# Optimization experiments

Measured on AMD Instinct MI355X. Metric: run time of the kernel, lower is better.

The kernel has to match this reference:

```python
import jax, jax.numpy as jnp
import numpy as np

B, S, I, H, L, O = 64, 512, 128, 1024, 3, 128


def _gru_cell(x, h, Wx, Wh, bh):
    # Wx: [3, H, in], Wh: [3, H, H], bh: [3, H]; gate order (z, r, g).
    # Matches: z = sig(W_xz x + W_hz h + b_z); r = sig(W_xr x + W_hr h + b_r);
    #          g = tanh(W_xg x + W_hg (r*h) + b_g); h' = z*h + (1-z)*g
    z = jax.nn.sigmoid(x @ Wx[0].T + h @ Wh[0].T + bh[0])
    r = jax.nn.sigmoid(x @ Wx[1].T + h @ Wh[1].T + bh[1])
    g = jnp.tanh(x @ Wx[2].T + (r * h) @ Wh[2].T + bh[2])
    return z * h + (1.0 - z) * g


def setup_inputs() -> dict:
    key = jax.random.key(0)
    ks = jax.random.split(key, 10)
    u = lambda k, shape, fan: jax.random.uniform(k, shape, jnp.float32, -1.0, 1.0) / np.float32(np.sqrt(fan))
    return {
        "x": jax.random.normal(ks[0], (B, S, I), jnp.float32),
        # layer 0 (input dim I)
        "Wx0": u(ks[1], (3, H, I), I),
        "Wh0": u(ks[2], (3, H, H), H),
        "bh0": u(ks[3], (3, H), H),
        # layers 1..L-1 (input dim H), stacked on leading axis
        "Wxr": u(ks[4], (L - 1, 3, H, H), H),
        "Whr": u(ks[5], (L - 1, 3, H, H), H),
        "bhr": u(ks[6], (L - 1, 3, H), H),
        # output projection
        "Wout": u(ks[7], (O, H), H),
        "bout": u(ks[8], (O,), H),
    }


def reference(x, Wx0, Wh0, bh0, Wxr, Whr, bhr, Wout, bout):
    batch = x.shape[0]
    n_rest = Wxr.shape[0]
    h_init = jnp.zeros((n_rest + 1, batch, H), x.dtype)  # [L, B, H]

    def step(hs, x_t):
        new = []
        h = _gru_cell(x_t, hs[0], Wx0, Wh0, bh0)
        new.append(h)
        inp = h
        for j in range(n_rest):  # small fixed layer count
            h = _gru_cell(inp, hs[j + 1], Wxr[j], Whr[j], bhr[j])
            new.append(h)
            inp = h
        y = inp @ Wout.T + bout
        return jnp.stack(new), y

    hs_final, ys = jax.lax.scan(step, h_init, jnp.swapaxes(x, 0, 1))
    layer_output = jnp.swapaxes(ys, 0, 1)        # (B, S, O)
    hidden_state = jnp.swapaxes(hs_final, 0, 1)  # (B, L, H)
    return layer_output, hidden_state
```

## Files before the change

### kernel.cpp

```cpp
#include <hip/hip_runtime.h>


namespace {
constexpr int kB = 64, kS = 512, kI = 128, kH = 1024, kO = 128;
constexpr int kTicks = kS + 3;
constexpr size_t kBSO = (size_t)kB * kS * kO;
constexpr int kTasksA = 218, kTasksB = 96;

__device__ float g_wxt0[3 * 128 * 1024];
__device__ float g_wht0[3 * 1024 * 1024];
__device__ float g_wxtr[6 * 1024 * 1024];
__device__ float g_whtr[6 * 1024 * 1024];
__device__ float g_woutT[1024 * 128];
__device__ float g_xT[512 * 128 * 64];
__device__ float g_hbuf[2 * 3 * 1024 * 64];
__device__ float g_zT[3 * 1024 * 64];
__device__ float g_rhT[3 * 1024 * 64];
__device__ float g_gxT[3 * 1024 * 64];
__device__ float g_partA[kTasksA * 8192];
__device__ float g_partB[kTasksB * 8192];
}


__global__ void zero_hbuf() {
  g_hbuf[blockIdx.x * 256 + threadIdx.x] = 0.f;
}

__global__ __launch_bounds__(256) void transpose_k(
    const float* __restrict__ in, int sel, int R, int C) {
  float* out;
  switch (sel) {
    case 0: out = g_wxt0; break;
    case 1: out = g_wht0; break;
    case 2: out = g_wxtr; break;
    case 3: out = g_whtr; break;
    case 4: out = g_woutT; break;
    default: out = g_xT; break;
  }
  const size_t mat = (size_t)R * C;
  in += blockIdx.z * mat;
  out += blockIdx.z * mat;
  __shared__ float t[32][33];
  const int c0 = blockIdx.x * 32, r0 = blockIdx.y * 32;
  const int tx = threadIdx.x & 31, ty = threadIdx.x >> 5;
  for (int i = ty; i < 32; i += 8) {
    const int r = r0 + i, c = c0 + tx;
    if (r < R && c < C) t[i][tx] = in[(size_t)r * C + c];
  }
  __syncthreads();
  for (int i = ty; i < 32; i += 8) {
    const int c = c0 + i, r = r0 + tx;
    if (c < C && r < R) out[(size_t)c * R + r] = t[tx][i];
  }
}

__device__ __forceinline__ void load_lds16(const float* g, float* l) {
  __builtin_amdgcn_global_load_lds(
      (const __attribute__((address_space(1))) void*)g,
      (__attribute__((address_space(3))) void*)l, 16, 0, 0);
}

__global__ __launch_bounds__(512) void gemm_tasks(int phase, int tau) {
  const int id = blockIdx.x;
  const int par = tau & 1;
  const float* hb = g_hbuf + par * 196608;

  int t_l = 0, nk = 512, ldw = 1024;
  const float* inp = nullptr; const float* w = nullptr;

  if (phase == 0) {
    if (id < 48) {
      const int gate = id / 24, q = id % 24, ng = q / 3, ks = q % 3;
      t_l = tau;
      if (ks == 0) {
        inp = g_xT + (size_t)t_l * 8192; nk = 128;
        w = g_wxt0 + (size_t)gate * 131072 + ng * 128;
      } else {
        const int k0 = (ks - 1) * 512;
        inp = hb + k0 * 64;
        w = g_wht0 + (size_t)gate * 1048576 + (size_t)k0 * 1024 + ng * 128;
      }
    } else if (id < 176) {
      const int q = id - 48, l = 1 + (q >> 6);
      const int q2 = q & 63, gate = q2 >> 5, q3 = q2 & 31, ng = q3 >> 2, ks = q3 & 3;
      t_l = tau - l;
      if (ks < 2) {
        const int k0 = ks * 512;
        inp = hb + (l - 1) * 65536 + k0 * 64;
        w = g_wxtr + (size_t)((l - 1) * 3 + gate) * 1048576 + (size_t)k0 * 1024 + ng * 128;
      } else {
        const int k0 = (ks - 2) * 512;
        inp = hb + l * 65536 + k0 * 64;
        w = g_whtr + (size_t)((l - 1) * 3 + gate) * 1048576 + (size_t)k0 * 1024 + ng * 128;
      }
    } else if (id < 184) {
      const int ng = id - 176;
      t_l = tau;
      inp = g_xT + (size_t)t_l * 8192; nk = 128;
      w = g_wxt0 + (size_t)2 * 131072 + ng * 128;
    } else if (id < 216) {
      const int q = id - 184, l = 1 + (q >> 4);
      const int q2 = q & 15, ng = q2 >> 1, ks = q2 & 1;
      t_l = tau - l;
      const int k0 = ks * 512;
      inp = hb + (l - 1) * 65536 + k0 * 64;
      w = g_wxtr + (size_t)((l - 1) * 3 + 2) * 1048576 + (size_t)k0 * 1024 + ng * 128;
    } else {
      const int ks = id - 216;
      t_l = tau - 3;
      const int k0 = ks * 512;
      inp = hb + 2 * 65536 + k0 * 64;
      w = g_woutT + (size_t)k0 * 128; ldw = 128;
    }
  } else {
    const int l = id >> 5, q = id & 31, ng = q >> 2, ks = q & 3;
    t_l = tau - l;
    const int k0 = ks * 256;
    inp = g_rhT + l * 65536 + k0 * 64; nk = 256;
    w = ((l == 0) ? g_wht0 + (size_t)2 * 1048576
                  : g_whtr + (size_t)((l - 1) * 3 + 2) * 1048576) +
        (size_t)k0 * 1024 + ng * 128;
  }
  if (t_l < 0 || t_l >= kS) return;

  __shared__ float sI[64 * 64];
  __shared__ float sW[64 * 128];
  const int tid = threadIdx.x;
  const int tn = (tid & 31) * 4, tb = (tid >> 5) * 4;
  float acc[4][4] = {};

  for (int c0 = 0; c0 < nk; c0 += 64) {
#pragma unroll
    for (int u = 0; u < 2; ++u) {
      const int idx = tid + u * 512;
      load_lds16(inp + c0 * 64 + idx * 4, sI + idx * 4);
    }
#pragma unroll
    for (int u = 0; u < 4; ++u) {
      const int idx = tid + u * 512, k = idx >> 5, f = idx & 31;
      load_lds16(w + (size_t)(c0 + k) * ldw + f * 4, sW + idx * 4);
    }
    __syncthreads();
#pragma unroll 8
    for (int k = 0; k < 64; ++k) {
      const float4 a = *(const float4*)(sI + k * 64 + tb);
      const float4 wv = *(const float4*)(sW + k * 128 + tn);
      acc[0][0] += wv.x * a.x; acc[0][1] += wv.x * a.y; acc[0][2] += wv.x * a.z; acc[0][3] += wv.x * a.w;
      acc[1][0] += wv.y * a.x; acc[1][1] += wv.y * a.y; acc[1][2] += wv.y * a.z; acc[1][3] += wv.y * a.w;
      acc[2][0] += wv.z * a.x; acc[2][1] += wv.z * a.y; acc[2][2] += wv.z * a.z; acc[2][3] += wv.z * a.w;
      acc[3][0] += wv.w * a.x; acc[3][1] += wv.w * a.y; acc[3][2] += wv.w * a.z; acc[3][3] += wv.w * a.w;
    }
    __syncthreads();
  }

  float* po = ((phase == 0) ? g_partA : g_partB) + (size_t)id * 8192;
#pragma unroll
  for (int i = 0; i < 4; ++i) {
    float4 v = {acc[i][0], acc[i][1], acc[i][2], acc[i][3]};
    *(float4*)(po + (tn + i) * 64 + tb) = v;
  }
}

__global__ __launch_bounds__(256) void reduceA(
    int tau, const float* __restrict__ Bh0, const float* __restrict__ Bhr,
    const float* __restrict__ Bout, float* __restrict__ Out) {
  const int gid = blockIdx.x * 256 + threadIdx.x;
  const int b0 = (gid & 15) * 4, c = gid >> 4;
  const int par = tau & 1;
  if (c < 6144) {
    const int gate = (c >= 3072) ? 1 : 0;
    const int cc = c - gate * 3072;
    const int l = cc >> 10, n = cc & 1023;
    const int t_l = tau - l;
    if (t_l < 0 || t_l >= kS) return;
    const int ng = n >> 7, cl = n & 127;
    int base, nks;
    if (l == 0) { base = gate * 24 + ng * 3;                  nks = 3; }
    else        { base = 48 + (l - 1) * 64 + gate * 32 + ng * 4; nks = 4; }
    const float bias = (l == 0) ? Bh0[gate * 1024 + n] : Bhr[(l - 1) * 3072 + gate * 1024 + n];
    float s0 = bias, s1 = bias, s2 = bias, s3 = bias;
    for (int j = 0; j < nks; ++j) {
      const float4 p = *(const float4*)&g_partA[(size_t)(base + j) * 8192 + cl * 64 + b0];
      s0 += p.x; s1 += p.y; s2 += p.z; s3 += p.w;
    }
    const float v0 = 1.f / (1.f + expf(-s0)), v1 = 1.f / (1.f + expf(-s1));
    const float v2 = 1.f / (1.f + expf(-s2)), v3 = 1.f / (1.f + expf(-s3));
    const int off = l * 65536 + n * 64 + b0;
    if (gate == 0) {
      *(float4*)&g_zT[off] = make_float4(v0, v1, v2, v3);
    } else {
      const float4 h = *(const float4*)&g_hbuf[par * 196608 + off];
      *(float4*)&g_rhT[off] = make_float4(v0 * h.x, v1 * h.y, v2 * h.z, v3 * h.w);
    }
  } else if (c < 9216) {
    const int cc = c - 6144, l = cc >> 10, n = cc & 1023;
    const int t_l = tau - l;
    if (t_l < 0 || t_l >= kS) return;
    const int ng = n >> 7, cl = n & 127;
    int base, nks;
    if (l == 0) { base = 176 + ng;                 nks = 1; }
    else        { base = 184 + (l - 1) * 16 + ng * 2; nks = 2; }
    const float bias = (l == 0) ? Bh0[2048 + n] : Bhr[(l - 1) * 3072 + 2048 + n];
    float s0 = bias, s1 = bias, s2 = bias, s3 = bias;
    for (int j = 0; j < nks; ++j) {
      const float4 p = *(const float4*)&g_partA[(size_t)(base + j) * 8192 + cl * 64 + b0];
      s0 += p.x; s1 += p.y; s2 += p.z; s3 += p.w;
    }
    *(float4*)&g_gxT[l * 65536 + n * 64 + b0] = make_float4(s0, s1, s2, s3);
  } else {
    const int o = c - 9216, ty = tau - 3;
    if (ty < 0 || ty >= kS) return;
    const float bias = Bout[o];
    float s0 = bias, s1 = bias, s2 = bias, s3 = bias;
    for (int j = 0; j < 2; ++j) {
      const float4 p = *(const float4*)&g_partA[(size_t)(216 + j) * 8192 + o * 64 + b0];
      s0 += p.x; s1 += p.y; s2 += p.z; s3 += p.w;
    }
    Out[((size_t)(b0 + 0) * kS + ty) * kO + o] = s0;
    Out[((size_t)(b0 + 1) * kS + ty) * kO + o] = s1;
    Out[((size_t)(b0 + 2) * kS + ty) * kO + o] = s2;
    Out[((size_t)(b0 + 3) * kS + ty) * kO + o] = s3;
  }
}

__global__ __launch_bounds__(256) void reduceB(
    int tau, float* __restrict__ Out) {
  const int gid = blockIdx.x * 256 + threadIdx.x;
  const int b0 = (gid & 15) * 4, c = gid >> 4;
  const int l = c >> 10, n = c & 1023;
  const int t_l = tau - l;
  if (t_l < 0 || t_l >= kS) return;
  const int par = tau & 1;
  const int ng = n >> 7, cl = n & 127;
  const int base = l * 32 + ng * 4;
  const int off = l * 65536 + n * 64 + b0;
  float4 gs = *(const float4*)&g_gxT[off];
  for (int j = 0; j < 4; ++j) {
    const float4 p = *(const float4*)&g_partB[(size_t)(base + j) * 8192 + cl * 64 + b0];
    gs.x += p.x; gs.y += p.y; gs.z += p.z; gs.w += p.w;
  }
  const float g0 = tanhf(gs.x), g1 = tanhf(gs.y), g2 = tanhf(gs.z), g3 = tanhf(gs.w);
  const float4 z = *(const float4*)&g_zT[off];
  const float4 h = *(const float4*)&g_hbuf[par * 196608 + off];
  float4 hn;
  hn.x = z.x * h.x + (1.f - z.x) * g0;
  hn.y = z.y * h.y + (1.f - z.y) * g1;
  hn.z = z.z * h.z + (1.f - z.z) * g2;
  hn.w = z.w * h.w + (1.f - z.w) * g3;
  *(float4*)&g_hbuf[(1 - par) * 196608 + off] = hn;
  if (t_l == kS - 1) {
    Out[kBSO + ((size_t)(b0 + 0) * 3 + l) * 1024 + n] = hn.x;
    Out[kBSO + ((size_t)(b0 + 1) * 3 + l) * 1024 + n] = hn.y;
    Out[kBSO + ((size_t)(b0 + 2) * 3 + l) * 1024 + n] = hn.z;
    Out[kBSO + ((size_t)(b0 + 3) * 3 + l) * 1024 + n] = hn.w;
  }
}

extern "C" void kernel_launch(void* const* d_in, const int* in_sizes, int n_in,
                              void* d_out, int out_size, void* d_ws, size_t ws_size,
                              hipStream_t stream) {
  const float* X    = (const float*)d_in[0];
  const float* Wx0  = (const float*)d_in[1];
  const float* Wh0  = (const float*)d_in[2];
  const float* bh0  = (const float*)d_in[3];
  const float* Wxr  = (const float*)d_in[4];
  const float* Whr  = (const float*)d_in[5];
  const float* bhr  = (const float*)d_in[6];
  const float* Wout = (const float*)d_in[7];
  const float* bout = (const float*)d_in[8];
  (void)d_ws; (void)ws_size;

  if (n_in != 9 ||
      in_sizes[0] != 64 * 512 * 128 || in_sizes[1] != 3 * 1024 * 128 ||
      in_sizes[2] != 3 * 1024 * 1024 || in_sizes[3] != 3 * 1024 ||
      in_sizes[4] != 2 * 3 * 1024 * 1024 || in_sizes[5] != 2 * 3 * 1024 * 1024 ||
      in_sizes[6] != 2 * 3 * 1024 || in_sizes[7] != 128 * 1024 ||
      in_sizes[8] != 128 || out_size != 64 * 512 * 128 + 64 * 3 * 1024)
    return;

  float* out = (float*)d_out;

  hipLaunchKernelGGL(zero_hbuf, dim3(1536), dim3(256), 0, stream);
  hipLaunchKernelGGL(transpose_k, dim3(4, 32, 3),   dim3(256), 0, stream, Wx0,  0, 1024, 128);
  hipLaunchKernelGGL(transpose_k, dim3(32, 32, 3),  dim3(256), 0, stream, Wh0,  1, 1024, 1024);
  hipLaunchKernelGGL(transpose_k, dim3(32, 32, 6),  dim3(256), 0, stream, Wxr,  2, 1024, 1024);
  hipLaunchKernelGGL(transpose_k, dim3(32, 32, 6),  dim3(256), 0, stream, Whr,  3, 1024, 1024);
  hipLaunchKernelGGL(transpose_k, dim3(32, 4, 1),   dim3(256), 0, stream, Wout, 4, 128, 1024);
  hipLaunchKernelGGL(transpose_k, dim3(2048, 2, 1), dim3(256), 0, stream, X,    5, 64, 65536);

  for (int tau = 0; tau < kTicks; ++tau) {
    hipLaunchKernelGGL(gemm_tasks, dim3(kTasksA), dim3(512), 0, stream, 0, tau);
    hipLaunchKernelGGL(reduceA, dim3(584), dim3(256), 0, stream,
                       tau, bh0, bhr, bout, out);
    if (tau < kTicks - 1) {
      hipLaunchKernelGGL(gemm_tasks, dim3(kTasksB), dim3(512), 0, stream, 1, tau);
      hipLaunchKernelGGL(reduceB, dim3(192), dim3(256), 0, stream, tau, out);
    }
  }
}
```

Measured before the change: 32.70 ms.

## Split GRU step GEMMs into finer K-split tasks and fuse gate reductions

Splits the per-tick gate GEMM into a dedicated gemmA with twice as many K-split tasks (256-thread blocks, 8x4 register tiles) and a gemmB that uses 64-wide column tiles with 8-way K-splits, giving more blocks per launch on the many-CU GPU. reduceA now only computes r*h, and reduceB fuses the z gate, the input-side g partials, the recurrent g partials and the output projection reduction. This removes the intermediate zT/gxT buffers. The cost is more partial sums to write and re-read and more blocks doing redundant setup.

```diff
diff --git a/kernel.cpp b/kernel.cpp
--- a/kernel.cpp
+++ b/kernel.cpp
@@ -5,7 +5,7 @@
 constexpr int kB = 64, kS = 512, kI = 128, kH = 1024, kO = 128;
 constexpr int kTicks = kS + 3;
 constexpr size_t kBSO = (size_t)kB * kS * kO;
-constexpr int kTasksA = 218, kTasksB = 96;
+constexpr int kTasksA = 412, kTasksB = 384;
 
 __device__ float g_wxt0[3 * 128 * 1024];
 __device__ float g_wht0[3 * 1024 * 1024];
@@ -14,11 +14,9 @@
 __device__ float g_woutT[1024 * 128];
 __device__ float g_xT[512 * 128 * 64];
 __device__ float g_hbuf[2 * 3 * 1024 * 64];
-__device__ float g_zT[3 * 1024 * 64];
 __device__ float g_rhT[3 * 1024 * 64];
-__device__ float g_gxT[3 * 1024 * 64];
 __device__ float g_partA[kTasksA * 8192];
-__device__ float g_partB[kTasksB * 8192];
+__device__ float g_partB[kTasksB * 4096];
 }
 
 
@@ -60,91 +58,136 @@
       (__attribute__((address_space(3))) void*)l, 16, 0, 0);
 }
 
-__global__ __launch_bounds__(512) void gemm_tasks(int phase, int tau) {
+__global__ __launch_bounds__(256) void gemmA(int tau) {
   const int id = blockIdx.x;
   const int par = tau & 1;
   const float* hb = g_hbuf + par * 196608;
 
-  int t_l = 0, nk = 512, ldw = 1024;
+  int t_l = 0, nk = 256, ldw = 1024;
   const float* inp = nullptr; const float* w = nullptr;
 
-  if (phase == 0) {
-    if (id < 48) {
-      const int gate = id / 24, q = id % 24, ng = q / 3, ks = q % 3;
-      t_l = tau;
-      if (ks == 0) {
-        inp = g_xT + (size_t)t_l * 8192; nk = 128;
-        w = g_wxt0 + (size_t)gate * 131072 + ng * 128;
-      } else {
-        const int k0 = (ks - 1) * 512;
-        inp = hb + k0 * 64;
-        w = g_wht0 + (size_t)gate * 1048576 + (size_t)k0 * 1024 + ng * 128;
-      }
-    } else if (id < 176) {
-      const int q = id - 48, l = 1 + (q >> 6);
-      const int q2 = q & 63, gate = q2 >> 5, q3 = q2 & 31, ng = q3 >> 2, ks = q3 & 3;
-      t_l = tau - l;
-      if (ks < 2) {
-        const int k0 = ks * 512;
-        inp = hb + (l - 1) * 65536 + k0 * 64;
-        w = g_wxtr + (size_t)((l - 1) * 3 + gate) * 1048576 + (size_t)k0 * 1024 + ng * 128;
-      } else {
-        const int k0 = (ks - 2) * 512;
-        inp = hb + l * 65536 + k0 * 64;
-        w = g_whtr + (size_t)((l - 1) * 3 + gate) * 1048576 + (size_t)k0 * 1024 + ng * 128;
-      }
-    } else if (id < 184) {
-      const int ng = id - 176;
-      t_l = tau;
+  if (id < 80) {
+    const int gate = id / 40, q = id % 40, ng = q / 5, ks = q % 5;
+    t_l = tau;
+    if (ks == 0) {
       inp = g_xT + (size_t)t_l * 8192; nk = 128;
-      w = g_wxt0 + (size_t)2 * 131072 + ng * 128;
-    } else if (id < 216) {
-      const int q = id - 184, l = 1 + (q >> 4);
-      const int q2 = q & 15, ng = q2 >> 1, ks = q2 & 1;
-      t_l = tau - l;
-      const int k0 = ks * 512;
+      w = g_wxt0 + (size_t)gate * 131072 + ng * 128;
+    } else {
+      const int k0 = (ks - 1) * 256;
+      inp = hb + k0 * 64;
+      w = g_wht0 + (size_t)gate * 1048576 + (size_t)k0 * 1024 + ng * 128;
+    }
+  } else if (id < 336) {
+    const int q = id - 80, l = 1 + (q >> 7);
+    const int q2 = q & 127, gate = q2 >> 6, q3 = q2 & 63, ng = q3 >> 3, ks = q3 & 7;
+    t_l = tau - l;
+    const int k0 = (ks & 3) * 256;
+    if (ks < 4) {
       inp = hb + (l - 1) * 65536 + k0 * 64;
-      w = g_wxtr + (size_t)((l - 1) * 3 + 2) * 1048576 + (size_t)k0 * 1024 + ng * 128;
+      w = g_wxtr + (size_t)((l - 1) * 3 + gate) * 1048576 + (size_t)k0 * 1024 + ng * 128;
     } else {
-      const int ks = id - 216;
-      t_l = tau - 3;
-      const int k0 = ks * 512;
-      inp = hb + 2 * 65536 + k0 * 64;
-      w = g_woutT + (size_t)k0 * 128; ldw = 128;
-    }
-  } else {
-    const int l = id >> 5, q = id & 31, ng = q >> 2, ks = q & 3;
+      inp = hb + l * 65536 + k0 * 64;
+      w = g_whtr + (size_t)((l - 1) * 3 + gate) * 1048576 + (size_t)k0 * 1024 + ng * 128;
+    }
+  } else if (id < 344) {
+    const int ng = id - 336;
+    t_l = tau;
+    inp = g_xT + (size_t)t_l * 8192; nk = 128;
+    w = g_wxt0 + (size_t)2 * 131072 + ng * 128;
+  } else if (id < 408) {
+    const int q = id - 344, l = 1 + (q >> 5);
+    const int q2 = q & 31, ng = q2 >> 2, ks = q2 & 3;
     t_l = tau - l;
     const int k0 = ks * 256;
-    inp = g_rhT + l * 65536 + k0 * 64; nk = 256;
-    w = ((l == 0) ? g_wht0 + (size_t)2 * 1048576
-                  : g_whtr + (size_t)((l - 1) * 3 + 2) * 1048576) +
-        (size_t)k0 * 1024 + ng * 128;
+    inp = hb + (l - 1) * 65536 + k0 * 64;
+    w = g_wxtr + (size_t)((l - 1) * 3 + 2) * 1048576 + (size_t)k0 * 1024 + ng * 128;
+  } else {
+    const int ks = id - 408;
+    t_l = tau - 3;
+    const int k0 = ks * 256;
+    inp = hb + 2 * 65536 + k0 * 64;
+    w = g_woutT + (size_t)k0 * 128; ldw = 128;
   }
   if (t_l < 0 || t_l >= kS) return;
 
   __shared__ float sI[64 * 64];
   __shared__ float sW[64 * 128];
   const int tid = threadIdx.x;
-  const int tn = (tid & 31) * 4, tb = (tid >> 5) * 4;
+  const int tn = (tid & 15) * 8, tb = (tid >> 4) * 4;
+  float acc[8][4] = {};
+
+  for (int c0 = 0; c0 < nk; c0 += 64) {
+#pragma unroll
+    for (int u = 0; u < 4; ++u) {
+      const int idx = tid + u * 256;
+      load_lds16(inp + c0 * 64 + idx * 4, sI + idx * 4);
+    }
+#pragma unroll
+    for (int u = 0; u < 8; ++u) {
+      const int idx = tid + u * 256, k = idx >> 5, f = idx & 31;
+      load_lds16(w + (size_t)(c0 + k) * ldw + f * 4, sW + idx * 4);
+    }
+    __syncthreads();
+#pragma unroll 4
+    for (int k = 0; k < 64; ++k) {
+      const float4 a = *(const float4*)(sI + k * 64 + tb);
+      const float4 w0 = *(const float4*)(sW + k * 128 + tn);
+      const float4 w1 = *(const float4*)(sW + k * 128 + tn + 4);
+      acc[0][0] += w0.x * a.x; acc[0][1] += w0.x * a.y; acc[0][2] += w0.x * a.z; acc[0][3] += w0.x * a.w;
+      acc[1][0] += w0.y * a.x; acc[1][1] += w0.y * a.y; acc[1][2] += w0.y * a.z; acc[1][3] += w0.y * a.w;
+      acc[2][0] += w0.z * a.x; acc[2][1] += w0.z * a.y; acc[2][2] += w0.z * a.z; acc[2][3] += w0.z * a.w;
+      acc[3][0] += w0.w * a.x; acc[3][1] += w0.w * a.y; acc[3][2] += w0.w * a.z; acc[3][3] += w0.w * a.w;
+      acc[4][0] += w1.x * a.x; acc[4][1] += w1.x * a.y; acc[4][2] += w1.x * a.z; acc[4][3] += w1.x * a.w;
+      acc[5][0] += w1.y * a.x; acc[5][1] += w1.y * a.y; acc[5][2] += w1.y * a.z; acc[5][3] += w1.y * a.w;
+      acc[6][0] += w1.z * a.x; acc[6][1] += w1.z * a.y; acc[6][2] += w1.z * a.z; acc[6][3] += w1.z * a.w;
+      acc[7][0] += w1.w * a.x; acc[7][1] += w1.w * a.y; acc[7][2] += w1.w * a.z; acc[7][3] += w1.w * a.w;
+    }
+    __syncthreads();
+  }
+
+  float* po = g_partA + (size_t)id * 8192;
+#pragma unroll
+  for (int i = 0; i < 8; ++i) {
+    float4 v = {acc[i][0], acc[i][1], acc[i][2], acc[i][3]};
+    *(float4*)(po + (tn + i) * 64 + tb) = v;
+  }
+}
+
+__global__ __launch_bounds__(256, 2) void gemmB(int tau) {
+  const int id = blockIdx.x;
+  const int l = id >> 7;
+  const int rem = id & 127, tile = rem >> 3, ks = rem & 7;
+  const int t_l = tau - l;
+  if (t_l < 0 || t_l >= kS) return;
+  const int k0 = ks * 128;
+  const float* inp = g_rhT + l * 65536 + k0 * 64;
+  const float* w =
+      ((l == 0) ? g_wht0 + (size_t)2 * 1048576
+                : g_whtr + (size_t)((l - 1) * 3 + 2) * 1048576) +
+      (size_t)k0 * 1024 + tile * 64;
+
+  __shared__ float sI[64 * 64];
+  __shared__ float sW[64 * 64];
+  const int tid = threadIdx.x;
+  const int tn = (tid & 15) * 4, tb = (tid >> 4) * 4;
   float acc[4][4] = {};
 
-  for (int c0 = 0; c0 < nk; c0 += 64) {
-#pragma unroll
-    for (int u = 0; u < 2; ++u) {
-      const int idx = tid + u * 512;
+  for (int c0 = 0; c0 < 128; c0 += 64) {
+#pragma unroll
+    for (int u = 0; u < 4; ++u) {
+      const int idx = tid + u * 256;
       load_lds16(inp + c0 * 64 + idx * 4, sI + idx * 4);
     }
 #pragma unroll
     for (int u = 0; u < 4; ++u) {
-      const int idx = tid + u * 512, k = idx >> 5, f = idx & 31;
-      load_lds16(w + (size_t)(c0 + k) * ldw + f * 4, sW + idx * 4);
+      const int idx = tid + u * 256, k = idx >> 4, f = idx & 15;
+      load_lds16(w + (size_t)(c0 + k) * 1024 + f * 4, sW + idx * 4);
     }
     __syncthreads();
 #pragma unroll 8
     for (int k = 0; k < 64; ++k) {
       const float4 a = *(const float4*)(sI + k * 64 + tb);
-      const float4 wv = *(const float4*)(sW + k * 128 + tn);
+      const float4 wv = *(const float4*)(sW + k * 64 + tn);
       acc[0][0] += wv.x * a.x; acc[0][1] += wv.x * a.y; acc[0][2] += wv.x * a.z; acc[0][3] += wv.x * a.w;
       acc[1][0] += wv.y * a.x; acc[1][1] += wv.y * a.y; acc[1][2] += wv.y * a.z; acc[1][3] += wv.y * a.w;
       acc[2][0] += wv.z * a.x; acc[2][1] += wv.z * a.y; acc[2][2] += wv.z * a.z; acc[2][3] += wv.z * a.w;
@@ -153,7 +196,7 @@
     __syncthreads();
   }
 
-  float* po = ((phase == 0) ? g_partA : g_partB) + (size_t)id * 8192;
+  float* po = g_partB + (size_t)id * 4096;
 #pragma unroll
   for (int i = 0; i < 4; ++i) {
     float4 v = {acc[i][0], acc[i][1], acc[i][2], acc[i][3]};
@@ -162,97 +205,95 @@
 }
 
 __global__ __launch_bounds__(256) void reduceA(
+    int tau, const float* __restrict__ Bh0, const float* __restrict__ Bhr) {
+  const int gid = blockIdx.x * 256 + threadIdx.x;
+  const int b0 = (gid & 15) * 4, c = gid >> 4;
+  const int par = tau & 1;
+  const int l = c >> 10, n = c & 1023;
+  const int t_l = tau - l;
+  if (t_l < 0 || t_l >= kS) return;
+  const int ng = n >> 7, cl = n & 127;
+  int base, nks;
+  if (l == 0) { base = 40 + ng * 5; nks = 5; }
+  else        { base = 80 + (l - 1) * 128 + 64 + ng * 8; nks = 8; }
+  const float bias = (l == 0) ? Bh0[1024 + n] : Bhr[(l - 1) * 3072 + 1024 + n];
+  float s0 = bias, s1 = bias, s2 = bias, s3 = bias;
+  for (int j = 0; j < nks; ++j) {
+    const float4 p = *(const float4*)&g_partA[(size_t)(base + j) * 8192 + cl * 64 + b0];
+    s0 += p.x; s1 += p.y; s2 += p.z; s3 += p.w;
+  }
+  const float v0 = 1.f / (1.f + expf(-s0)), v1 = 1.f / (1.f + expf(-s1));
+  const float v2 = 1.f / (1.f + expf(-s2)), v3 = 1.f / (1.f + expf(-s3));
+  const int off = l * 65536 + n * 64 + b0;
+  const float4 h = *(const float4*)&g_hbuf[par * 196608 + off];
+  *(float4*)&g_rhT[off] = make_float4(v0 * h.x, v1 * h.y, v2 * h.z, v3 * h.w);
+}
+
+__global__ __launch_bounds__(256) void reduceB(
     int tau, const float* __restrict__ Bh0, const float* __restrict__ Bhr,
     const float* __restrict__ Bout, float* __restrict__ Out) {
   const int gid = blockIdx.x * 256 + threadIdx.x;
   const int b0 = (gid & 15) * 4, c = gid >> 4;
   const int par = tau & 1;
-  if (c < 6144) {
-    const int gate = (c >= 3072) ? 1 : 0;
-    const int cc = c - gate * 3072;
-    const int l = cc >> 10, n = cc & 1023;
+  if (c < 3072) {
+    const int l = c >> 10, n = c & 1023;
     const int t_l = tau - l;
     if (t_l < 0 || t_l >= kS) return;
     const int ng = n >> 7, cl = n & 127;
-    int base, nks;
-    if (l == 0) { base = gate * 24 + ng * 3;                  nks = 3; }
-    else        { base = 48 + (l - 1) * 64 + gate * 32 + ng * 4; nks = 4; }
-    const float bias = (l == 0) ? Bh0[gate * 1024 + n] : Bhr[(l - 1) * 3072 + gate * 1024 + n];
-    float s0 = bias, s1 = bias, s2 = bias, s3 = bias;
-    for (int j = 0; j < nks; ++j) {
-      const float4 p = *(const float4*)&g_partA[(size_t)(base + j) * 8192 + cl * 64 + b0];
-      s0 += p.x; s1 += p.y; s2 += p.z; s3 += p.w;
-    }
-    const float v0 = 1.f / (1.f + expf(-s0)), v1 = 1.f / (1.f + expf(-s1));
-    const float v2 = 1.f / (1.f + expf(-s2)), v3 = 1.f / (1.f + expf(-s3));
+    int zbase, znks;
+    if (l == 0) { zbase = ng * 5; znks = 5; }
+    else        { zbase = 80 + (l - 1) * 128 + ng * 8; znks = 8; }
+    const float zb = (l == 0) ? Bh0[n] : Bhr[(l - 1) * 3072 + n];
+    float z0 = zb, z1 = zb, z2 = zb, z3 = zb;
+    for (int j = 0; j < znks; ++j) {
+      const float4 p = *(const float4*)&g_partA[(size_t)(zbase + j) * 8192 + cl * 64 + b0];
+      z0 += p.x; z1 += p.y; z2 += p.z; z3 += p.w;
+    }
+    z0 = 1.f / (1.f + expf(-z0)); z1 = 1.f / (1.f + expf(-z1));
+    z2 = 1.f / (1.f + expf(-z2)); z3 = 1.f / (1.f + expf(-z3));
+    int gxbase, gxn;
+    if (l == 0) { gxbase = 336 + ng; gxn = 1; }
+    else        { gxbase = 344 + (l - 1) * 32 + ng * 4; gxn = 4; }
+    const float gb = (l == 0) ? Bh0[2048 + n] : Bhr[(l - 1) * 3072 + 2048 + n];
+    float g0 = gb, g1 = gb, g2 = gb, g3 = gb;
+    for (int j = 0; j < gxn; ++j) {
+      const float4 p = *(const float4*)&g_partA[(size_t)(gxbase + j) * 8192 + cl * 64 + b0];
+      g0 += p.x; g1 += p.y; g2 += p.z; g3 += p.w;
+    }
+    const int tile64 = n >> 6, cl64 = n & 63;
+    const int ghbase = l * 128 + tile64 * 8;
+    for (int j = 0; j < 8; ++j) {
+      const float4 p = *(const float4*)&g_partB[(size_t)(ghbase + j) * 4096 + cl64 * 64 + b0];
+      g0 += p.x; g1 += p.y; g2 += p.z; g3 += p.w;
+    }
+    g0 = tanhf(g0); g1 = tanhf(g1); g2 = tanhf(g2); g3 = tanhf(g3);
     const int off = l * 65536 + n * 64 + b0;
-    if (gate == 0) {
-      *(float4*)&g_zT[off] = make_float4(v0, v1, v2, v3);
-    } else {
-      const float4 h = *(const float4*)&g_hbuf[par * 196608 + off];
-      *(float4*)&g_rhT[off] = make_float4(v0 * h.x, v1 * h.y, v2 * h.z, v3 * h.w);
-    }
-  } else if (c < 9216) {
-    const int cc = c - 6144, l = cc >> 10, n = cc & 1023;
-    const int t_l = tau - l;
-    if (t_l < 0 || t_l >= kS) return;
-    const int ng = n >> 7, cl = n & 127;
-    int base, nks;
-    if (l == 0) { base = 176 + ng;                 nks = 1; }
-    else        { base = 184 + (l - 1) * 16 + ng * 2; nks = 2; }
-    const float bias = (l == 0) ? Bh0[2048 + n] : Bhr[(l - 1) * 3072 + 2048 + n];
-    float s0 = bias, s1 = bias, s2 = bias, s3 = bias;
-    for (int j = 0; j < nks; ++j) {
-      const float4 p = *(const float4*)&g_partA[(size_t)(base + j) * 8192 + cl * 64 + b0];
-      s0 += p.x; s1 += p.y; s2 += p.z; s3 += p.w;
-    }
-    *(float4*)&g_gxT[l * 65536 + n * 64 + b0] = make_float4(s0, s1, s2, s3);
+    const float4 h = *(const float4*)&g_hbuf[par * 196608 + off];
+    float4 hn;
+    hn.x = z0 * h.x + (1.f - z0) * g0;
+    hn.y = z1 * h.y + (1.f - z1) * g1;
+    hn.z = z2 * h.z + (1.f - z2) * g2;
+    hn.w = z3 * h.w + (1.f - z3) * g3;
+    *(float4*)&g_hbuf[(1 - par) * 196608 + off] = hn;
+    if (t_l == kS - 1) {
+      Out[kBSO + ((size_t)(b0 + 0) * 3 + l) * 1024 + n] = hn.x;
+      Out[kBSO + ((size_t)(b0 + 1) * 3 + l) * 1024 + n] = hn.y;
+      Out[kBSO + ((size_t)(b0 + 2) * 3 + l) * 1024 + n] = hn.z;
+      Out[kBSO + ((size_t)(b0 + 3) * 3 + l) * 1024 + n] = hn.w;
+    }
   } else {
-    const int o = c - 9216, ty = tau - 3;
+    const int o = c - 3072, ty = tau - 3;
     if (ty < 0 || ty >= kS) return;
     const float bias = Bout[o];
     float s0 = bias, s1 = bias, s2 = bias, s3 = bias;
-    for (int j = 0; j < 2; ++j) {
-      const float4 p = *(const float4*)&g_partA[(size_t)(216 + j) * 8192 + o * 64 + b0];
+    for (int j = 0; j < 4; ++j) {
+      const float4 p = *(const float4*)&g_partA[(size_t)(408 + j) * 8192 + o * 64 + b0];
       s0 += p.x; s1 += p.y; s2 += p.z; s3 += p.w;
     }
     Out[((size_t)(b0 + 0) * kS + ty) * kO + o] = s0;
     Out[((size_t)(b0 + 1) * kS + ty) * kO + o] = s1;
     Out[((size_t)(b0 + 2) * kS + ty) * kO + o] = s2;
     Out[((size_t)(b0 + 3) * kS + ty) * kO + o] = s3;
-  }
-}
-
-__global__ __launch_bounds__(256) void reduceB(
-    int tau, float* __restrict__ Out) {
-  const int gid = blockIdx.x * 256 + threadIdx.x;
-  const int b0 = (gid & 15) * 4, c = gid >> 4;
-  const int l = c >> 10, n = c & 1023;
-  const int t_l = tau - l;
-  if (t_l < 0 || t_l >= kS) return;
-  const int par = tau & 1;
-  const int ng = n >> 7, cl = n & 127;
-  const int base = l * 32 + ng * 4;
-  const int off = l * 65536 + n * 64 + b0;
-  float4 gs = *(const float4*)&g_gxT[off];
-  for (int j = 0; j < 4; ++j) {
-    const float4 p = *(const float4*)&g_partB[(size_t)(base + j) * 8192 + cl * 64 + b0];
-    gs.x += p.x; gs.y += p.y; gs.z += p.z; gs.w += p.w;
-  }
-  const float g0 = tanhf(gs.x), g1 = tanhf(gs.y), g2 = tanhf(gs.z), g3 = tanhf(gs.w);
-  const float4 z = *(const float4*)&g_zT[off];
-  const float4 h = *(const float4*)&g_hbuf[par * 196608 + off];
-  float4 hn;
-  hn.x = z.x * h.x + (1.f - z.x) * g0;
-  hn.y = z.y * h.y + (1.f - z.y) * g1;
-  hn.z = z.z * h.z + (1.f - z.z) * g2;
-  hn.w = z.w * h.w + (1.f - z.w) * g3;
-  *(float4*)&g_hbuf[(1 - par) * 196608 + off] = hn;
-  if (t_l == kS - 1) {
-    Out[kBSO + ((size_t)(b0 + 0) * 3 + l) * 1024 + n] = hn.x;
-    Out[kBSO + ((size_t)(b0 + 1) * 3 + l) * 1024 + n] = hn.y;
-    Out[kBSO + ((size_t)(b0 + 2) * 3 + l) * 1024 + n] = hn.z;
-    Out[kBSO + ((size_t)(b0 + 3) * 3 + l) * 1024 + n] = hn.w;
   }
 }
 
@@ -289,12 +330,11 @@
   hipLaunchKernelGGL(transpose_k, dim3(2048, 2, 1), dim3(256), 0, stream, X,    5, 64, 65536);
 
   for (int tau = 0; tau < kTicks; ++tau) {
-    hipLaunchKernelGGL(gemm_tasks, dim3(kTasksA), dim3(512), 0, stream, 0, tau);
-    hipLaunchKernelGGL(reduceA, dim3(584), dim3(256), 0, stream,
+    hipLaunchKernelGGL(gemmA, dim3(kTasksA), dim3(256), 0, stream, tau);
+    hipLaunchKernelGGL(reduceA, dim3(192), dim3(256), 0, stream, tau, bh0, bhr);
+    if (tau < kTicks - 1)
+      hipLaunchKernelGGL(gemmB, dim3(kTasksB), dim3(256), 0, stream, tau);
+    hipLaunchKernelGGL(reduceB, dim3(200), dim3(256), 0, stream,
                        tau, bh0, bhr, bout, out);
-    if (tau < kTicks - 1) {
-      hipLaunchKernelGGL(gemm_tasks, dim3(kTasksB), dim3(512), 0, stream, 1, tau);
-      hipLaunchKernelGGL(reduceB, dim3(192), dim3(256), 0, stream, tau, out);
-    }
-  }
-}
+  }
+}
```

New measurement: 27.28 ms. 16.6% less time.
